# Kernel tuning notes

Hardware: AMD Instinct MI355X
Metric: run time of the kernel (lower is better)

## Reference

```python
import jax, jax.numpy as jnp
import numpy as np

B = 8192          # batch_size
NB = 4096         # num_banks (== mask length)
PAD = NB // 2     # reflect pad on each side


def setup_inputs() -> dict:
    key = jax.random.key(0)
    k1, k2, k3 = jax.random.split(key, 3)
    logits = jax.random.normal(k1, (NB,), dtype=jnp.float32) * 0.1
    u = jax.random.uniform(k2, (B, NB), dtype=jnp.float32)          # Bernoulli uniforms
    shift = jax.random.randint(k3, (B,), 0, NB, dtype=jnp.int32)    # per-sample shift
    return {"logits": logits, "u": u, "shift": shift}


def reference(logits, u, shift):
    # Bernoulli(sigmoid(logits)) sample via inverse-CDF on externally supplied uniforms
    p = jax.nn.sigmoid(logits)                       # (NB,)
    grid = (u < p).astype(jnp.float32)               # (B, NB)
    # Bernoulli log_prob summed over banks: g*log(p) + (1-g)*log(1-p)
    log_probs = (grid * jax.nn.log_sigmoid(logits)
                 + (1.0 - grid) * jax.nn.log_sigmoid(-logits)).sum(axis=1)  # (B,)
    # reflect-pad along bank axis, then gather a shifted window of length NB
    padded = jnp.pad(grid, ((0, 0), (PAD, PAD)), mode="reflect")    # (B, NB+2*PAD)
    idx = shift[:, None].astype(jnp.int32) + jnp.arange(NB, dtype=jnp.int32)[None, :]
    masks = jnp.take_along_axis(padded, idx, axis=1)[:, None, :]    # (B, 1, NB)
    return masks, log_probs
```

## Files before the change

### kernel.cpp

```cpp
#include <hip/hip_runtime.h>
#include <math.h>

#define NB 4096
#define PAD 2048
#define BLOCK 256
#define V4 (NB / 4 / BLOCK)

__device__ __forceinline__ int mirror_idx(int i) {
    i = ::abs(i);
    return (i < NB) ? i : (2 * (NB - 1) - i);
}

__global__ void fbmp_precompute(const float* __restrict__ logits, float* __restrict__ ws) {
    __shared__ float sred[BLOCK / 64];
    float lsnsum = 0.0f;
    for (int j = threadIdx.x; j < NB; j += BLOCK) {
        float x = logits[j];
        double xd = (double)x;
        float e = (float)exp(-xd);
        float p = 1.0f / (1.0f + e);
        float lsp = (float)(-log1p(exp(-xd)));
        float lsn = (float)(-log1p(exp(xd)));
        ws[j] = p;
        ws[NB + j] = lsp - lsn;
        lsnsum += lsn;
    }
    #pragma unroll
    for (int off = 32; off > 0; off >>= 1)
        lsnsum += __shfl_down(lsnsum, off, 64);
    const int lane = threadIdx.x & 63;
    const int wid  = threadIdx.x >> 6;
    if (lane == 0) sred[wid] = lsnsum;
    __syncthreads();
    if (threadIdx.x == 0) {
        float t = 0.0f;
        #pragma unroll
        for (int w = 0; w < BLOCK / 64; ++w) t += sred[w];
        ws[2 * NB] = t;
    }
}

__global__ __launch_bounds__(BLOCK) void fbmp_main(
    const float* __restrict__ u, const int* __restrict__ shift,
    const float* __restrict__ ws,
    float* __restrict__ masks, float* __restrict__ logp)
{
    __shared__ float sg[NB];
    __shared__ float sred[BLOCK / 64];

    const int b = blockIdx.x;
    const int t = threadIdx.x;
    const float4* __restrict__ u4 = (const float4*)(u + (size_t)b * NB);
    const float4* __restrict__ p4 = (const float4*)ws;
    const float4* __restrict__ d4 = (const float4*)(ws + NB);
    const int s = shift[b] - PAD;

    float4 uv[V4], pv[V4], dv[V4];
    #pragma unroll
    for (int i = 0; i < V4; ++i) uv[i] = u4[t + i * BLOCK];
    #pragma unroll
    for (int i = 0; i < V4; ++i) pv[i] = p4[t + i * BLOCK];
    #pragma unroll
    for (int i = 0; i < V4; ++i) dv[i] = d4[t + i * BLOCK];

    float acc = 0.0f;
    #pragma unroll
    for (int i = 0; i < V4; ++i) {
        bool c0 = uv[i].x < pv[i].x;
        bool c1 = uv[i].y < pv[i].y;
        bool c2 = uv[i].z < pv[i].z;
        bool c3 = uv[i].w < pv[i].w;
        acc += (c0 ? dv[i].x : 0.0f) + (c1 ? dv[i].y : 0.0f)
             + (c2 ? dv[i].z : 0.0f) + (c3 ? dv[i].w : 0.0f);
        float4 g;
        g.x = c0 ? 1.0f : 0.0f;
        g.y = c1 ? 1.0f : 0.0f;
        g.z = c2 ? 1.0f : 0.0f;
        g.w = c3 ? 1.0f : 0.0f;
        ((float4*)sg)[t + i * BLOCK] = g;
    }
    __syncthreads();

    float4* __restrict__ m4 = (float4*)(masks + (size_t)b * NB);
    #pragma unroll
    for (int i = 0; i < V4; ++i) {
        const int k = 4 * (t + i * BLOCK) + s;
        float4 o;
        o.x = sg[mirror_idx(k + 0)];
        o.y = sg[mirror_idx(k + 1)];
        o.z = sg[mirror_idx(k + 2)];
        o.w = sg[mirror_idx(k + 3)];
        m4[t + i * BLOCK] = o;
    }

    #pragma unroll
    for (int off = 32; off > 0; off >>= 1)
        acc += __shfl_down(acc, off, 64);
    const int lane = t & 63;
    const int wid  = t >> 6;
    if (lane == 0) sred[wid] = acc;
    __syncthreads();
    if (t == 0) {
        float tot = 0.0f;
        #pragma unroll
        for (int w = 0; w < BLOCK / 64; ++w) tot += sred[w];
        logp[b] = tot + ws[2 * NB];
    }
}

extern "C" void kernel_launch(void* const* d_in, const int* in_sizes, int n_in,
                              void* d_out, int out_size, void* d_ws, size_t ws_size,
                              hipStream_t stream) {
    const float* logits = (const float*)d_in[0];
    const float* u      = (const float*)d_in[1];
    const int*   shift  = (const int*)d_in[2];
    const int B = in_sizes[2];

    float* ws    = (float*)d_ws;
    float* masks = (float*)d_out;
    float* logp  = (float*)d_out + (size_t)B * NB;

    fbmp_precompute<<<1, BLOCK, 0, stream>>>(logits, ws);
    fbmp_main<<<B, BLOCK, 0, stream>>>(u, shift, ws, masks, logp);
}
```

Baseline: 247.3 us.

## Process four rows per block with register prefetch and double-buffered LDS

Each block now handles four consecutive rows with 512 threads, loading the next row's uniforms into registers while the current row is compared, written to LDS and gathered. The LDS buffer is double-buffered so only one barrier is needed per row, and that barrier is a custom waitcnt+s_barrier. Probability and delta vectors are loaded once per block and reused across rows. The aim is more memory-level parallelism and less per-block overhead, at the cost of higher register use and fewer blocks.

```diff
diff --git a/kernel.cpp b/kernel.cpp
--- a/kernel.cpp
+++ b/kernel.cpp
@@ -3,18 +3,24 @@
 
 #define NB 4096
 #define PAD 2048
-#define BLOCK 256
+#define BLOCK 512
 #define V4 (NB / 4 / BLOCK)
+#define ROWS 4
+#define PBLOCK 256
 
 __device__ __forceinline__ int mirror_idx(int i) {
     i = ::abs(i);
     return (i < NB) ? i : (2 * (NB - 1) - i);
 }
 
+__device__ __forceinline__ void lds_barrier() {
+    asm volatile("s_waitcnt lgkmcnt(0)\n\ts_barrier" ::: "memory");
+}
+
 __global__ void fbmp_precompute(const float* __restrict__ logits, float* __restrict__ ws) {
-    __shared__ float sred[BLOCK / 64];
+    __shared__ float sred[PBLOCK / 64];
     float lsnsum = 0.0f;
-    for (int j = threadIdx.x; j < NB; j += BLOCK) {
+    for (int j = threadIdx.x; j < NB; j += PBLOCK) {
         float x = logits[j];
         double xd = (double)x;
         float e = (float)exp(-xd);
@@ -35,76 +41,98 @@
     if (threadIdx.x == 0) {
         float t = 0.0f;
         #pragma unroll
-        for (int w = 0; w < BLOCK / 64; ++w) t += sred[w];
+        for (int w = 0; w < PBLOCK / 64; ++w) t += sred[w];
         ws[2 * NB] = t;
     }
 }
 
-__global__ __launch_bounds__(BLOCK) void fbmp_main(
+__global__ __launch_bounds__(BLOCK, 8) void fbmp_main(
     const float* __restrict__ u, const int* __restrict__ shift,
     const float* __restrict__ ws,
     float* __restrict__ masks, float* __restrict__ logp)
 {
-    __shared__ float sg[NB];
-    __shared__ float sred[BLOCK / 64];
+    __shared__ float sg[2][NB];
+    __shared__ float sred[ROWS][BLOCK / 64];
 
     const int b = blockIdx.x;
     const int t = threadIdx.x;
-    const float4* __restrict__ u4 = (const float4*)(u + (size_t)b * NB);
+    const int row0 = b * ROWS;
+
     const float4* __restrict__ p4 = (const float4*)ws;
     const float4* __restrict__ d4 = (const float4*)(ws + NB);
-    const int s = shift[b] - PAD;
-
-    float4 uv[V4], pv[V4], dv[V4];
-    #pragma unroll
-    for (int i = 0; i < V4; ++i) uv[i] = u4[t + i * BLOCK];
+    float4 pv[V4], dv[V4];
     #pragma unroll
     for (int i = 0; i < V4; ++i) pv[i] = p4[t + i * BLOCK];
     #pragma unroll
     for (int i = 0; i < V4; ++i) dv[i] = d4[t + i * BLOCK];
+    const float base = ws[2 * NB];
 
-    float acc = 0.0f;
-    #pragma unroll
-    for (int i = 0; i < V4; ++i) {
-        bool c0 = uv[i].x < pv[i].x;
-        bool c1 = uv[i].y < pv[i].y;
-        bool c2 = uv[i].z < pv[i].z;
-        bool c3 = uv[i].w < pv[i].w;
-        acc += (c0 ? dv[i].x : 0.0f) + (c1 ? dv[i].y : 0.0f)
-             + (c2 ? dv[i].z : 0.0f) + (c3 ? dv[i].w : 0.0f);
-        float4 g;
-        g.x = c0 ? 1.0f : 0.0f;
-        g.y = c1 ? 1.0f : 0.0f;
-        g.z = c2 ? 1.0f : 0.0f;
-        g.w = c3 ? 1.0f : 0.0f;
-        ((float4*)sg)[t + i * BLOCK] = g;
-    }
-    __syncthreads();
-
-    float4* __restrict__ m4 = (float4*)(masks + (size_t)b * NB);
-    #pragma unroll
-    for (int i = 0; i < V4; ++i) {
-        const int k = 4 * (t + i * BLOCK) + s;
-        float4 o;
-        o.x = sg[mirror_idx(k + 0)];
-        o.y = sg[mirror_idx(k + 1)];
-        o.z = sg[mirror_idx(k + 2)];
-        o.w = sg[mirror_idx(k + 3)];
-        m4[t + i * BLOCK] = o;
+    float4 ucur[V4], unext[V4];
+    {
+        const float4* __restrict__ u0 = (const float4*)(u + (size_t)row0 * NB);
+        #pragma unroll
+        for (int i = 0; i < V4; ++i) ucur[i] = u0[t + i * BLOCK];
     }
 
     #pragma unroll
-    for (int off = 32; off > 0; off >>= 1)
-        acc += __shfl_down(acc, off, 64);
-    const int lane = t & 63;
-    const int wid  = t >> 6;
-    if (lane == 0) sred[wid] = acc;
-    __syncthreads();
+    for (int r = 0; r < ROWS; ++r) {
+        if (r + 1 < ROWS) {
+            const float4* __restrict__ un =
+                (const float4*)(u + (size_t)(row0 + r + 1) * NB);
+            #pragma unroll
+            for (int i = 0; i < V4; ++i) unext[i] = un[t + i * BLOCK];
+        }
+        const int s = shift[row0 + r] - PAD;
+
+        float* __restrict__ buf = sg[r & 1];
+        float acc = 0.0f;
+        #pragma unroll
+        for (int i = 0; i < V4; ++i) {
+            bool c0 = ucur[i].x < pv[i].x;
+            bool c1 = ucur[i].y < pv[i].y;
+            bool c2 = ucur[i].z < pv[i].z;
+            bool c3 = ucur[i].w < pv[i].w;
+            acc += (c0 ? dv[i].x : 0.0f) + (c1 ? dv[i].y : 0.0f)
+                 + (c2 ? dv[i].z : 0.0f) + (c3 ? dv[i].w : 0.0f);
+            float4 g;
+            g.x = c0 ? 1.0f : 0.0f;
+            g.y = c1 ? 1.0f : 0.0f;
+            g.z = c2 ? 1.0f : 0.0f;
+            g.w = c3 ? 1.0f : 0.0f;
+            ((float4*)buf)[t + i * BLOCK] = g;
+        }
+
+        #pragma unroll
+        for (int off = 32; off > 0; off >>= 1)
+            acc += __shfl_down(acc, off, 64);
+        if ((t & 63) == 0) sred[r][t >> 6] = acc;
+
+        lds_barrier();
+
+        float4* __restrict__ m4 = (float4*)(masks + (size_t)(row0 + r) * NB);
+        #pragma unroll
+        for (int i = 0; i < V4; ++i) {
+            const int k = 4 * (t + i * BLOCK) + s;
+            float4 o;
+            o.x = buf[mirror_idx(k + 0)];
+            o.y = buf[mirror_idx(k + 1)];
+            o.z = buf[mirror_idx(k + 2)];
+            o.w = buf[mirror_idx(k + 3)];
+            m4[t + i * BLOCK] = o;
+        }
+
+        #pragma unroll
+        for (int i = 0; i < V4; ++i) ucur[i] = unext[i];
+    }
+
     if (t == 0) {
-        float tot = 0.0f;
         #pragma unroll
-        for (int w = 0; w < BLOCK / 64; ++w) tot += sred[w];
-        logp[b] = tot + ws[2 * NB];
+        for (int r = 0; r < ROWS; ++r) {
+            float tot = 0.0f;
+            #pragma unroll
+            for (int w = 0; w < BLOCK / 64; ++w) tot += sred[r][w];
+            logp[row0 + r] = tot + base;
+        }
     }
 }
 
@@ -120,6 +148,6 @@
     float* masks = (float*)d_out;
     float* logp  = (float*)d_out + (size_t)B * NB;
 
-    fbmp_precompute<<<1, BLOCK, 0, stream>>>(logits, ws);
-    fbmp_main<<<B, BLOCK, 0, stream>>>(u, shift, ws, masks, logp);
+    fbmp_precompute<<<1, PBLOCK, 0, stream>>>(logits, ws);
+    fbmp_main<<<B / ROWS, BLOCK, 0, stream>>>(u, shift, ws, masks, logp);
 }
```

After: 254.6 us. +3.0%, slower.
